# Kernel optimization log

Hardware: AMD Instinct MI355X
Metric: run time of the kernel (lower is better)

Reference implementation:

```python
import jax, jax.numpy as jnp
import numpy as np

G = 10            # int(2 / 0.2) BEV grid side
NUM_PILLARS = G * G
INTERVAL = 0.2
BN_EPS = 1e-5


def setup_inputs() -> dict:
    key = jax.random.key(0)
    ks = jax.random.split(key, 8)
    B, N = 8, 20000
    x = jax.random.normal(ks[0], (B, N, 3), dtype=jnp.float32)
    # Linear weights stored as [in, out] (torch Linear applies x @ W.T); no biases.
    W1 = jax.random.normal(ks[1], (6, 32), dtype=jnp.float32) * 0.1
    W2 = jax.random.normal(ks[2], (32, 64), dtype=jnp.float32) * 0.1
    W3 = jax.random.normal(ks[3], (64, 128), dtype=jnp.float32) * 0.1
    W4 = jax.random.normal(ks[4], (256, 768), dtype=jnp.float32) * 0.05
    bn_gamma = jnp.ones((NUM_PILLARS,), dtype=jnp.float32)
    bn_beta = jnp.zeros((NUM_PILLARS,), dtype=jnp.float32)
    return {"x": x, "W1": W1, "W2": W2, "W3": W3, "W4": W4,
            "bn_gamma": bn_gamma, "bn_beta": bn_beta}


def _encode_sample(p, seg, W1, W2, W3, W4):
    # p: [N,3] swapped coords (Z,Y,X); seg: [N] pillar id in [0,100)
    N = p.shape[0]
    counts = jax.ops.segment_sum(jnp.ones((N,), p.dtype), seg, num_segments=NUM_PILLARS)  # [100]
    cent = jax.ops.segment_sum(p, seg, num_segments=NUM_PILLARS) / jnp.maximum(counts, 1.0)[:, None]
    aug = jnp.concatenate([p, p - cent[seg]], axis=-1)          # [N,6]
    h = jax.nn.relu(aug @ W1)
    h = jax.nn.relu(h @ W2)
    h = jax.nn.relu(h @ W3)                                      # [N,128]
    pil = jax.ops.segment_max(h, seg, num_segments=NUM_PILLARS)  # [100,128] (-inf on empty, never gathered)
    h2 = jnp.concatenate([h, pil[seg]], axis=-1)                 # [N,256]
    h2 = jax.nn.relu(h2 @ W4)                                    # [N,768]
    enc = jax.ops.segment_max(h2, seg, num_segments=NUM_PILLARS) # [100,768]
    return jnp.where(counts[:, None] > 0, enc, 0.0)             # empty pillars stay zero


def reference(x, W1, W2, W3, W4, bn_gamma, bn_beta):
    # column swap [Y,Z,X] -> [Z,Y,X]
    pts = jnp.stack([x[..., 1], x[..., 0], x[..., 2]], axis=-1)  # [B,N,3]
    # pillar indices from (Y, X) = swapped cols 1:3
    yx = jnp.clip(pts[..., 1:] + 1.0, 0.0, 1.99)
    idx = jnp.floor(yx / INTERVAL).astype(jnp.int32)             # trunc == floor (non-negative)
    seg = idx[..., 0] * G + idx[..., 1]                          # [B,N], matches flatten(2) order y*10+x
    feat = jax.vmap(lambda p, s: _encode_sample(p, s, W1, W2, W3, W4))(pts, seg)  # [B,100,768]
    # BatchNorm1d(100) in training mode over [B, 100, 768]: stats over dims (0,2)
    mean = feat.mean(axis=(0, 2))
    var = feat.var(axis=(0, 2))  # biased variance, as torch uses for normalization
    out = (feat - mean[None, :, None]) * jax.lax.rsqrt(var + BN_EPS)[None, :, None]
    return out * bn_gamma[None, :, None] + bn_beta[None, :, None]
```

## Files before the change

### kernel.cpp

```cpp
#include <hip/hip_runtime.h>
#include <stdint.h>

#define B_    8
#define N_    20000
#define NPTS  (B_*N_)
#define G_    10
#define NPIL  100
#define NSB   (B_*NPIL)
#define BN_EPS 1e-5f

#define OFF_COUNTS   0
#define OFF_SUMS     3200
#define OFF_STARTS   12800
#define OFF_ZPAD     16064
#define ZERO_BYTES   16320
#define OFF_CENT     19264
#define OFF_SEG      28864
#define OFF_W3BF     668864
#define OFF_W4T      709824
#define OFF_PILBF    1103040
#define OFF_PILW4B   1307840
#define OFF_H3P      3765440
#define WS_NEED      44725440

typedef __attribute__((ext_vector_type(8))) short bf16x8;
typedef __attribute__((ext_vector_type(4))) float f32x4;

typedef const __attribute__((address_space(1))) void gas_void;
typedef __attribute__((address_space(3))) void las_void;

__device__ __forceinline__ void gload_lds16(const void* g, void* l){
    __builtin_amdgcn_global_load_lds((gas_void*)g, (las_void*)l, 16, 0, 0);
}

__device__ __forceinline__ int binidx(float v){
    float t = v + 1.0f;
    t = fminf(fmaxf(t, 0.0f), 1.99f);
    return (int)(t / 0.2f);
}
__device__ __forceinline__ unsigned short f2bf(float f){
    unsigned u = __float_as_uint(f);
    u += 0x7fffu + ((u >> 16) & 1u);
    return (unsigned short)(u >> 16);
}
__device__ __forceinline__ unsigned u16max2(unsigned a, unsigned b){
    unsigned ah=a>>16, bh=b>>16, al=a&0xffffu, bl=b&0xffffu;
    return ((ah>bh?ah:bh)<<16) | (al>bl?al:bl);
}
__device__ __forceinline__ uint4 max16(uint4 a, uint4 b){
    uint4 r; r.x=u16max2(a.x,b.x); r.y=u16max2(a.y,b.y);
    r.z=u16max2(a.z,b.z); r.w=u16max2(a.w,b.w); return r;
}

__global__ __launch_bounds__(256) void kA(const float* __restrict__ x,
                                          int* __restrict__ segrank,
                                          int* __restrict__ counts,
                                          float* __restrict__ sums){
    __shared__ int   lc[NSB];
    __shared__ float lsum[NSB*3];
    __shared__ int   lbase[NSB];
    int tid = threadIdx.x;
    for (int j = tid; j < NSB; j += 256){
        lc[j] = 0;
        lsum[3*j] = 0.f; lsum[3*j+1] = 0.f; lsum[3*j+2] = 0.f;
    }
    __syncthreads();
    int i0 = blockIdx.x * 625;
    int sbv[3], lrv[3];
    #pragma unroll
    for (int t = 0; t < 3; t++){
        int i = i0 + tid + t*256;
        sbv[t] = -1;
        if (tid + t*256 < 625 && i < NPTS){
            float x0 = x[3*i], x1 = x[3*i+1], x2 = x[3*i+2];
            int b  = i / N_;
            int sb = b*NPIL + binidx(x0)*G_ + binidx(x2);
            sbv[t] = sb;
            lrv[t] = atomicAdd(&lc[sb], 1);
            atomicAdd(&lsum[sb*3+0], x1);
            atomicAdd(&lsum[sb*3+1], x0);
            atomicAdd(&lsum[sb*3+2], x2);
        }
    }
    __syncthreads();
    for (int j = tid; j < NSB; j += 256){
        int c = lc[j];
        if (c > 0){
            lbase[j] = atomicAdd(&counts[j], c);
            atomicAdd(&sums[3*j+0], lsum[3*j+0]);
            atomicAdd(&sums[3*j+1], lsum[3*j+1]);
            atomicAdd(&sums[3*j+2], lsum[3*j+2]);
        }
    }
    __syncthreads();
    #pragma unroll
    for (int t = 0; t < 3; t++){
        if (sbv[t] >= 0){
            int i = i0 + tid + t*256;
            int rank = lbase[sbv[t]] + lrv[t];
            segrank[i] = sbv[t] | (rank << 10);
        }
    }
}

__global__ __launch_bounds__(1024) void kScan(const int* __restrict__ counts,
                                              int* __restrict__ starts){
    __shared__ int s[1024];
    int t = threadIdx.x;
    int c = (t < NSB) ? counts[t] : 0;
    s[t] = c;
    __syncthreads();
    for (int off=1; off<1024; off<<=1){
        int v = (t >= off) ? s[t-off] : 0;
        __syncthreads();
        s[t] += v;
        __syncthreads();
    }
    if (t < NSB) starts[t] = s[t]-c;
    if (t == NSB) starts[NSB] = s[NSB-1];
}

__global__ __launch_bounds__(256) void kB(const int* __restrict__ counts,
                                          const float* __restrict__ sums,
                                          float* __restrict__ cent,
                                          const float* __restrict__ W3,
                                          unsigned short* __restrict__ W3bf,
                                          const float* __restrict__ W4,
                                          unsigned short* __restrict__ W4T){
    int idx = blockIdx.x*256 + threadIdx.x;
    if (idx < 2400){
        cent[idx] = sums[idx] / fmaxf((float)counts[idx/3], 1.0f);
    } else if (idx < 2400 + 8192){
        int t = idx - 2400;
        int col = t >> 6, k = t & 63;
        W3bf[t] = f2bf(W3[k*128 + col]);
    } else if (idx < 2400 + 8192 + 196608){
        int t = idx - 2400 - 8192;
        int k = t / 768, j = t - k*768;
        W4T[j*256 + k] = f2bf(W4[t]);
    }
}

__global__ __launch_bounds__(256) void kC12(const float* __restrict__ x,
                                            const int* __restrict__ segrank,
                                            const int* __restrict__ starts,
                                            const float* __restrict__ cent,
                                            const float* __restrict__ W1,
                                            const float* __restrict__ W2,
                                            unsigned short* __restrict__ h3p){
    int i = blockIdx.x*256 + threadIdx.x;
    if (i >= NPTS) return;
    int pk = segrank[i];
    int sb = pk & 1023;
    int pos = starts[sb] + (pk >> 10);
    float p0 = x[3*i+1], p1 = x[3*i], p2 = x[3*i+2];
    float aug[6];
    aug[0]=p0; aug[1]=p1; aug[2]=p2;
    aug[3]=p0-cent[sb*3+0]; aug[4]=p1-cent[sb*3+1]; aug[5]=p2-cent[sb*3+2];

    float h1[32];
    #pragma unroll
    for (int j=0;j<32;j++){
        float a = 0.f;
        #pragma unroll
        for (int k=0;k<6;k++) a += aug[k]*W1[k*32+j];
        h1[j] = fmaxf(a, 0.f);
    }
    unsigned buf[32];
    #pragma unroll 8
    for (int jp=0;jp<32;jp++){
        float a0 = 0.f, a1 = 0.f;
        #pragma unroll
        for (int k=0;k<32;k++){
            a0 += h1[k]*W2[k*64 + jp*2];
            a1 += h1[k]*W2[k*64 + jp*2 + 1];
        }
        buf[jp] = (unsigned)f2bf(fmaxf(a0,0.f)) | ((unsigned)f2bf(fmaxf(a1,0.f)) << 16);
    }
    uint4* d4 = (uint4*)(h3p + (size_t)pos*128 + 64);
    #pragma unroll
    for (int q=0;q<8;q++) d4[q] = ((const uint4*)buf)[q];
}

__global__ __launch_bounds__(512) void kC3(const unsigned short* __restrict__ W3bf,
                                           unsigned short* __restrict__ h3p){
    __shared__ unsigned short Al[256*64];
    __shared__ unsigned short Bl[128*64];
    int tid = threadIdx.x;
    int m0  = blockIdx.x * 256;
    #pragma unroll
    for (int it=0; it<4; it++){
        int cc = tid + it*512;
        int row = cc >> 3, ch = cc & 7;
        int chs = ch ^ (row & 7);
        gload_lds16(h3p + (size_t)(m0+row)*128 + 64 + chs*8, (char*)Al + cc*16);
    }
    #pragma unroll
    for (int it=0; it<2; it++){
        int cc = tid + it*512;
        int row = cc >> 3, ch = cc & 7;
        int chs = ch ^ (row & 7);
        gload_lds16(W3bf + (size_t)row*64 + chs*8, (char*)Bl + cc*16);
    }
    __syncthreads();

    int lane = tid & 63, wid = tid >> 6;
    int wm = wid >> 1, wn = wid & 1;
    int l15 = lane & 15, lhi = lane >> 4;

    f32x4 acc[4][4];
    #pragma unroll
    for (int m=0;m<4;m++)
        #pragma unroll
        for (int n=0;n<4;n++) acc[m][n] = (f32x4){0.f,0.f,0.f,0.f};

    #pragma unroll
    for (int kk=0; kk<2; kk++){
        bf16x8 af[4], bfr[4];
        #pragma unroll
        for (int f=0; f<4; f++){
            int ra = wm*64 + f*16 + l15;
            af[f]  = *(const bf16x8*)((char*)Al + ra*128 + (((kk*4+lhi) ^ (ra&7))*16));
            int rb = wn*64 + f*16 + l15;
            bfr[f] = *(const bf16x8*)((char*)Bl + rb*128 + (((kk*4+lhi) ^ (rb&7))*16));
        }
        #pragma unroll
        for (int m=0;m<4;m++)
            #pragma unroll
            for (int n=0;n<4;n++)
                acc[m][n] = __builtin_amdgcn_mfma_f32_16x16x32_bf16(af[m], bfr[n], acc[m][n], 0,0,0);
    }

    #pragma unroll
    for (int m=0;m<4;m++)
        #pragma unroll
        for (int r=0;r<4;r++){
            int row = m0 + wm*64 + m*16 + lhi*4 + r;
            #pragma unroll
            for (int n=0;n<4;n++){
                int col = wn*64 + n*16 + l15;
                h3p[(size_t)row*128 + col] = f2bf(fmaxf(acc[m][n][r], 0.f));
            }
        }
}

__global__ __launch_bounds__(256) void kM(const unsigned short* __restrict__ h3p,
                                          const int* __restrict__ starts,
                                          unsigned short* __restrict__ pilbf){
    __shared__ uint4 sd[16][16];
    int sb = blockIdx.x;
    int tx = threadIdx.x & 15, ty = threadIdx.x >> 4;
    int s = starts[sb], npts = starts[sb+1] - s;
    uint4 acc = {0u,0u,0u,0u};
    for (int p = ty; p < npts; p += 16){
        uint4 v = *(const uint4*)(h3p + (size_t)(s+p)*128 + tx*8);
        acc = max16(acc, v);
    }
    sd[ty][tx] = acc;
    __syncthreads();
    #pragma unroll
    for (int off=8; off; off>>=1){
        if (ty < off) sd[ty][tx] = max16(sd[ty][tx], sd[ty+off][tx]);
        __syncthreads();
    }
    if (ty == 0) *(uint4*)(pilbf + sb*128 + tx*8) = sd[0][tx];
}

__global__ __launch_bounds__(256) void kPB(const unsigned short* __restrict__ pilbf,
                                           const unsigned short* __restrict__ W4T,
                                           float* __restrict__ pilW4b){
    __shared__ unsigned short Al[128*128];
    __shared__ unsigned short Bl[128*128];
    int m0 = blockIdx.x * 128;
    int n0 = blockIdx.y * 128;
    int tid = threadIdx.x;
    #pragma unroll
    for (int it=0; it<8; it++){
        int cc = tid + it*256;
        int row = cc >> 4, ch = cc & 15;
        int chs = ch ^ (row & 7);
        uint4 v = {0u,0u,0u,0u};
        if (m0 + row < NSB) v = *(const uint4*)(pilbf + (size_t)(m0+row)*128 + chs*8);
        *(uint4*)((char*)Al + cc*16) = v;
        uint4 vb = *(const uint4*)(W4T + (size_t)(n0+row)*256 + 128 + chs*8);
        *(uint4*)((char*)Bl + cc*16) = vb;
    }
    __syncthreads();
    int lane = tid & 63, wid = tid >> 6;
    int wm = wid >> 1, wn = wid & 1;
    int l15 = lane & 15, lhi = lane >> 4;
    f32x4 acc[4][4];
    #pragma unroll
    for (int m=0;m<4;m++)
        #pragma unroll
        for (int n=0;n<4;n++) acc[m][n] = (f32x4){0.f,0.f,0.f,0.f};
    #pragma unroll
    for (int kk=0; kk<4; kk++){
        bf16x8 af[4], bfr[4];
        #pragma unroll
        for (int f=0; f<4; f++){
            int ra = wm*64 + f*16 + l15;
            af[f]  = *(const bf16x8*)((char*)Al + ra*256 + (((kk*4+lhi) ^ (ra&7))*16));
            int rb = wn*64 + f*16 + l15;
            bfr[f] = *(const bf16x8*)((char*)Bl + rb*256 + (((kk*4+lhi) ^ (rb&7))*16));
        }
        #pragma unroll
        for (int m=0;m<4;m++)
            #pragma unroll
            for (int n=0;n<4;n++)
                acc[m][n] = __builtin_amdgcn_mfma_f32_16x16x32_bf16(af[m], bfr[n], acc[m][n], 0,0,0);
    }
    #pragma unroll
    for (int m=0;m<4;m++)
        #pragma unroll
        for (int r=0;r<4;r++){
            int p = wm*64 + m*16 + lhi*4 + r;
            int sbp = m0 + p;
            if (sbp < NSB){
                #pragma unroll
                for (int n=0;n<4;n++)
                    pilW4b[(size_t)sbp*768 + n0 + wn*64 + n*16 + l15] = acc[m][n][r];
            }
        }
}

__global__ __launch_bounds__(256) void kD(const unsigned short* __restrict__ h3p,
                                          const unsigned short* __restrict__ zpad,
                                          const int* __restrict__ starts,
                                          const float* __restrict__ pilW4b,
                                          const unsigned short* __restrict__ W4T,
                                          float* __restrict__ out){
    __shared__ unsigned short Al[128*128];
    __shared__ unsigned short Bl[128*128];
    __shared__ float red[2][2][64];
    int b  = blockIdx.x;
    int x_ = b & 7, t_ = b >> 3;
    int k_ = t_ / 6, nt = t_ - k_*6;
    int sb = x_ + 8*k_;
    int n0 = nt * 128;
    int tid = threadIdx.x;
    int start = starts[sb];
    int npts  = starts[sb+1] - start;
    if (npts == 0){
        if (tid < 128) out[(size_t)sb*768 + n0 + tid] = 0.f;
        return;
    }
    #pragma unroll
    for (int it=0; it<8; it++){
        int cc = tid + it*256;
        int row = cc >> 4, ch = cc & 15;
        int chs = ch ^ (row & 7);
        gload_lds16(W4T + (size_t)(n0+row)*256 + chs*8, (char*)Bl + cc*16);
    }
    int lane = tid & 63, wid = tid >> 6;
    int wm = wid >> 1, wn = wid & 1;
    int l15 = lane & 15, lhi = lane >> 4;

    float bias[4];
    #pragma unroll
    for (int n=0;n<4;n++) bias[n] = pilW4b[(size_t)sb*768 + n0 + wn*64 + n*16 + l15];

    float mx[4][4][4];
    #pragma unroll
    for (int m=0;m<4;m++)
        #pragma unroll
        for (int n=0;n<4;n++)
            #pragma unroll
            for (int r=0;r<4;r++) mx[m][n][r] = 0.f;

    int nch = (npts + 127) >> 7;
    for (int c=0; c<nch; c++){
        int base = c*128;
        __syncthreads();
        #pragma unroll
        for (int it=0; it<8; it++){
            int cc = tid + it*256;
            int row = cc >> 4, ch = cc & 15;
            int chs = ch ^ (row & 7);
            const unsigned short* src = (base + row < npts)
                ? h3p + (size_t)(start+base+row)*128 + chs*8
                : zpad + chs*8;
            gload_lds16(src, (char*)Al + cc*16);
        }
        __syncthreads();

        f32x4 acc[4][4];
        #pragma unroll
        for (int m=0;m<4;m++)
            #pragma unroll
            for (int n=0;n<4;n++) acc[m][n] = (f32x4){0.f,0.f,0.f,0.f};

        #pragma unroll
        for (int kk=0; kk<4; kk++){
            bf16x8 af[4], bfr[4];
            #pragma unroll
            for (int f=0; f<4; f++){
                int ra = wm*64 + f*16 + l15;
                af[f]  = *(const bf16x8*)((char*)Al + ra*256 + (((kk*4+lhi) ^ (ra&7))*16));
                int rb = wn*64 + f*16 + l15;
                bfr[f] = *(const bf16x8*)((char*)Bl + rb*256 + (((kk*4+lhi) ^ (rb&7))*16));
            }
            #pragma unroll
            for (int m=0;m<4;m++)
                #pragma unroll
                for (int n=0;n<4;n++)
                    acc[m][n] = __builtin_amdgcn_mfma_f32_16x16x32_bf16(af[m], bfr[n], acc[m][n], 0,0,0);
        }

        int nrem = npts - base;
        #pragma unroll
        for (int m=0;m<4;m++)
            #pragma unroll
            for (int r=0;r<4;r++){
                int p = wm*64 + m*16 + lhi*4 + r;
                if (p < nrem){
                    #pragma unroll
                    for (int n=0;n<4;n++)
                        mx[m][n][r] = fmaxf(mx[m][n][r], fmaxf(acc[m][n][r] + bias[n], 0.f));
                }
            }
    }

    float red4[4];
    #pragma unroll
    for (int n=0;n<4;n++){
        float v = 0.f;
        #pragma unroll
        for (int m=0;m<4;m++)
            #pragma unroll
            for (int r=0;r<4;r++) v = fmaxf(v, mx[m][n][r]);
        v = fmaxf(v, __shfl_xor(v, 16));
        v = fmaxf(v, __shfl_xor(v, 32));
        red4[n] = v;
    }
    if (lhi == 0){
        #pragma unroll
        for (int n=0;n<4;n++) red[wm][wn][n*16 + l15] = red4[n];
    }
    __syncthreads();
    if (wm == 0){
        float v = fmaxf(red[0][wn][lane], red[1][wn][lane]);
        out[(size_t)sb*768 + n0 + wn*64 + lane] = v;
    }
}

__global__ __launch_bounds__(256) void kE(float* __restrict__ out,
                                          const float* __restrict__ gamma,
                                          const float* __restrict__ beta){
    int p = blockIdx.x;
    int tid = threadIdx.x;
    float v[B_*3];
    float sum = 0.f, ssq = 0.f;
    #pragma unroll
    for (int b=0;b<B_;b++)
        #pragma unroll
        for (int r=0;r<3;r++){
            float t = out[(b*NPIL + p)*768 + tid + r*256];
            v[b*3+r] = t;
            sum += t; ssq += t*t;
        }
    #pragma unroll
    for (int off=32; off; off>>=1){
        sum += __shfl_xor(sum, off);
        ssq += __shfl_xor(ssq, off);
    }
    __shared__ float ls[8];
    __shared__ float sc[2];
    int lane = tid & 63, w = tid >> 6;
    if (lane == 0){ ls[w] = sum; ls[4+w] = ssq; }
    __syncthreads();
    if (tid == 0){
        float S = ls[0]+ls[1]+ls[2]+ls[3];
        float Q = ls[4]+ls[5]+ls[6]+ls[7];
        float mean = S * (1.0f/6144.0f);
        float var  = Q * (1.0f/6144.0f) - mean*mean;
        float scale = rsqrtf(var + BN_EPS) * gamma[p];
        sc[0] = scale;
        sc[1] = beta[p] - mean*scale;
    }
    __syncthreads();
    float scale = sc[0], shift = sc[1];
    #pragma unroll
    for (int b=0;b<B_;b++)
        #pragma unroll
        for (int r=0;r<3;r++)
            out[(b*NPIL + p)*768 + tid + r*256] = v[b*3+r]*scale + shift;
}

extern "C" void kernel_launch(void* const* d_in, const int* in_sizes, int n_in,
                              void* d_out, int out_size, void* d_ws, size_t ws_size,
                              hipStream_t stream){
    if (ws_size < (size_t)WS_NEED) return;
    const float* x     = (const float*)d_in[0];
    const float* W1    = (const float*)d_in[1];
    const float* W2    = (const float*)d_in[2];
    const float* W3    = (const float*)d_in[3];
    const float* W4    = (const float*)d_in[4];
    const float* gamma = (const float*)d_in[5];
    const float* beta  = (const float*)d_in[6];
    float* out = (float*)d_out;
    char*  ws  = (char*)d_ws;

    int*            counts = (int*)           (ws + OFF_COUNTS);
    float*          sums   = (float*)         (ws + OFF_SUMS);
    int*            starts = (int*)           (ws + OFF_STARTS);
    unsigned short* zpad   = (unsigned short*)(ws + OFF_ZPAD);
    float*          cent   = (float*)         (ws + OFF_CENT);
    int*            segrank= (int*)           (ws + OFF_SEG);
    unsigned short* W3bf   = (unsigned short*)(ws + OFF_W3BF);
    unsigned short* W4T    = (unsigned short*)(ws + OFF_W4T);
    unsigned short* pilbf  = (unsigned short*)(ws + OFF_PILBF);
    float*          pilW4b = (float*)         (ws + OFF_PILW4B);
    unsigned short* h3p    = (unsigned short*)(ws + OFF_H3P);

    hipMemsetAsync(d_ws, 0, ZERO_BYTES, stream);

    kA<<<256, 256, 0, stream>>>(x, segrank, counts, sums);
    kScan<<<1, 1024, 0, stream>>>(counts, starts);
    kB<<<(2400+8192+196608+255)/256, 256, 0, stream>>>(counts, sums, cent, W3, W3bf, W4, W4T);
    kC12<<<(NPTS+255)/256, 256, 0, stream>>>(x, segrank, starts, cent, W1, W2, h3p);
    kC3<<<NPTS/256, 512, 0, stream>>>(W3bf, h3p);
    kM<<<NSB, 256, 0, stream>>>(h3p, starts, pilbf);
    dim3 gPB((NSB+127)/128, 6);
    kPB<<<gPB, 256, 0, stream>>>(pilbf, W4T, pilW4b);
    kD<<<4800, 256, 0, stream>>>(h3p, zpad, starts, pilW4b, W4T, out);
    kE<<<NPIL, 256, 0, stream>>>(out, gamma, beta);
}
```

Before: 175.7 us.

## Fuse layer-3 MFMA into per-point MLP kernel and pillar max/bias into kD

Merges the per-point layer 1-2 kernel with the layer-3 MFMA GEMM, so the 64-wide intermediate goes through LDS and no longer round-trips through h3p in global memory. It also drops the separate pillar segment-max and pillar-bias GEMM kernels. Each kD block now recomputes the pillar max over its points and a 128-column slice of the pillar·W4 bias in scalar code. This removes three launches and global round trips, but the 6 column-tile blocks per pillar repeat the max reduction and bias dot products, and the fused kernel raises register and LDS use.

```diff
diff --git a/kernel.cpp b/kernel.cpp
--- a/kernel.cpp
+++ b/kernel.cpp
@@ -18,8 +18,6 @@
 #define OFF_SEG      28864
 #define OFF_W3BF     668864
 #define OFF_W4T      709824
-#define OFF_PILBF    1103040
-#define OFF_PILW4B   1307840
 #define OFF_H3P      3765440
 #define WS_NEED      44725440
 
@@ -141,18 +139,33 @@
     }
 }
 
-__global__ __launch_bounds__(256) void kC12(const float* __restrict__ x,
-                                            const int* __restrict__ segrank,
-                                            const int* __restrict__ starts,
-                                            const float* __restrict__ cent,
-                                            const float* __restrict__ W1,
-                                            const float* __restrict__ W2,
-                                            unsigned short* __restrict__ h3p){
-    int i = blockIdx.x*256 + threadIdx.x;
-    if (i >= NPTS) return;
+__global__ __launch_bounds__(256) void kCF(const float* __restrict__ x,
+                                           const int* __restrict__ segrank,
+                                           const int* __restrict__ starts,
+                                           const float* __restrict__ cent,
+                                           const float* __restrict__ W1,
+                                           const float* __restrict__ W2,
+                                           const unsigned short* __restrict__ W3bf,
+                                           unsigned short* __restrict__ h3p){
+    __shared__ uint4 Hl4[256*8];
+    __shared__ uint4 Bw4[128*8];
+    __shared__ int posl[256];
+    unsigned short* Hl = (unsigned short*)Hl4;
+    unsigned short* Bw = (unsigned short*)Bw4;
+    int tid = threadIdx.x;
+    int i = blockIdx.x*256 + tid;
     int pk = segrank[i];
     int sb = pk & 1023;
-    int pos = starts[sb] + (pk >> 10);
+    posl[tid] = starts[sb] + (pk >> 10);
+
+    #pragma unroll
+    for (int it=0; it<4; it++){
+        int cc = tid + it*256;
+        int row = cc >> 3, ch = cc & 7;
+        int chs = ch ^ (row & 7);
+        gload_lds16(W3bf + (size_t)row*64 + chs*8, (char*)Bw + cc*16);
+    }
+
     float p0 = x[3*i+1], p1 = x[3*i], p2 = x[3*i+2];
     float aug[6];
     aug[0]=p0; aug[1]=p1; aug[2]=p2;
@@ -166,7 +179,7 @@
         for (int k=0;k<6;k++) a += aug[k]*W1[k*32+j];
         h1[j] = fmaxf(a, 0.f);
     }
-    unsigned buf[32];
+    unsigned buf[32] __attribute__((aligned(16)));
     #pragma unroll 8
     for (int jp=0;jp<32;jp++){
         float a0 = 0.f, a1 = 0.f;
@@ -177,30 +190,10 @@
         }
         buf[jp] = (unsigned)f2bf(fmaxf(a0,0.f)) | ((unsigned)f2bf(fmaxf(a1,0.f)) << 16);
     }
-    uint4* d4 = (uint4*)(h3p + (size_t)pos*128 + 64);
-    #pragma unroll
-    for (int q=0;q<8;q++) d4[q] = ((const uint4*)buf)[q];
-}
-
-__global__ __launch_bounds__(512) void kC3(const unsigned short* __restrict__ W3bf,
-                                           unsigned short* __restrict__ h3p){
-    __shared__ unsigned short Al[256*64];
-    __shared__ unsigned short Bl[128*64];
-    int tid = threadIdx.x;
-    int m0  = blockIdx.x * 256;
-    #pragma unroll
-    for (int it=0; it<4; it++){
-        int cc = tid + it*512;
-        int row = cc >> 3, ch = cc & 7;
-        int chs = ch ^ (row & 7);
-        gload_lds16(h3p + (size_t)(m0+row)*128 + 64 + chs*8, (char*)Al + cc*16);
-    }
-    #pragma unroll
-    for (int it=0; it<2; it++){
-        int cc = tid + it*512;
-        int row = cc >> 3, ch = cc & 7;
-        int chs = ch ^ (row & 7);
-        gload_lds16(W3bf + (size_t)row*64 + chs*8, (char*)Bl + cc*16);
+    #pragma unroll
+    for (int ch=0; ch<8; ch++){
+        int chs = ch ^ (tid & 7);
+        *(uint4*)((char*)Hl + tid*128 + chs*16) = ((const uint4*)buf)[ch];
     }
     __syncthreads();
 
@@ -208,131 +201,56 @@
     int wm = wid >> 1, wn = wid & 1;
     int l15 = lane & 15, lhi = lane >> 4;
 
-    f32x4 acc[4][4];
-    #pragma unroll
-    for (int m=0;m<4;m++)
-        #pragma unroll
-        for (int n=0;n<4;n++) acc[m][n] = (f32x4){0.f,0.f,0.f,0.f};
+    f32x4 acc[8][4];
+    #pragma unroll
+    for (int f=0;f<8;f++)
+        #pragma unroll
+        for (int n=0;n<4;n++) acc[f][n] = (f32x4){0.f,0.f,0.f,0.f};
 
     #pragma unroll
     for (int kk=0; kk<2; kk++){
-        bf16x8 af[4], bfr[4];
-        #pragma unroll
-        for (int f=0; f<4; f++){
-            int ra = wm*64 + f*16 + l15;
-            af[f]  = *(const bf16x8*)((char*)Al + ra*128 + (((kk*4+lhi) ^ (ra&7))*16));
-            int rb = wn*64 + f*16 + l15;
-            bfr[f] = *(const bf16x8*)((char*)Bl + rb*128 + (((kk*4+lhi) ^ (rb&7))*16));
-        }
-        #pragma unroll
-        for (int m=0;m<4;m++)
+        bf16x8 af[8], bfr[4];
+        #pragma unroll
+        for (int f=0; f<8; f++){
+            int ra = wm*128 + f*16 + l15;
+            af[f] = *(const bf16x8*)((char*)Hl + ra*128 + (((kk*4+lhi) ^ (ra&7))*16));
+        }
+        #pragma unroll
+        for (int n=0; n<4; n++){
+            int rb = wn*64 + n*16 + l15;
+            bfr[n] = *(const bf16x8*)((char*)Bw + rb*128 + (((kk*4+lhi) ^ (rb&7))*16));
+        }
+        #pragma unroll
+        for (int f=0;f<8;f++)
             #pragma unroll
             for (int n=0;n<4;n++)
-                acc[m][n] = __builtin_amdgcn_mfma_f32_16x16x32_bf16(af[m], bfr[n], acc[m][n], 0,0,0);
-    }
-
-    #pragma unroll
-    for (int m=0;m<4;m++)
+                acc[f][n] = __builtin_amdgcn_mfma_f32_16x16x32_bf16(af[f], bfr[n], acc[f][n], 0,0,0);
+    }
+
+    #pragma unroll
+    for (int f=0;f<8;f++)
         #pragma unroll
         for (int r=0;r<4;r++){
-            int row = m0 + wm*64 + m*16 + lhi*4 + r;
-            #pragma unroll
-            for (int n=0;n<4;n++){
-                int col = wn*64 + n*16 + l15;
-                h3p[(size_t)row*128 + col] = f2bf(fmaxf(acc[m][n][r], 0.f));
-            }
-        }
-}
-
-__global__ __launch_bounds__(256) void kM(const unsigned short* __restrict__ h3p,
-                                          const int* __restrict__ starts,
-                                          unsigned short* __restrict__ pilbf){
-    __shared__ uint4 sd[16][16];
-    int sb = blockIdx.x;
-    int tx = threadIdx.x & 15, ty = threadIdx.x >> 4;
-    int s = starts[sb], npts = starts[sb+1] - s;
-    uint4 acc = {0u,0u,0u,0u};
-    for (int p = ty; p < npts; p += 16){
-        uint4 v = *(const uint4*)(h3p + (size_t)(s+p)*128 + tx*8);
-        acc = max16(acc, v);
-    }
-    sd[ty][tx] = acc;
-    __syncthreads();
-    #pragma unroll
-    for (int off=8; off; off>>=1){
-        if (ty < off) sd[ty][tx] = max16(sd[ty][tx], sd[ty+off][tx]);
-        __syncthreads();
-    }
-    if (ty == 0) *(uint4*)(pilbf + sb*128 + tx*8) = sd[0][tx];
-}
-
-__global__ __launch_bounds__(256) void kPB(const unsigned short* __restrict__ pilbf,
-                                           const unsigned short* __restrict__ W4T,
-                                           float* __restrict__ pilW4b){
-    __shared__ unsigned short Al[128*128];
-    __shared__ unsigned short Bl[128*128];
-    int m0 = blockIdx.x * 128;
-    int n0 = blockIdx.y * 128;
-    int tid = threadIdx.x;
-    #pragma unroll
-    for (int it=0; it<8; it++){
-        int cc = tid + it*256;
-        int row = cc >> 4, ch = cc & 15;
-        int chs = ch ^ (row & 7);
-        uint4 v = {0u,0u,0u,0u};
-        if (m0 + row < NSB) v = *(const uint4*)(pilbf + (size_t)(m0+row)*128 + chs*8);
-        *(uint4*)((char*)Al + cc*16) = v;
-        uint4 vb = *(const uint4*)(W4T + (size_t)(n0+row)*256 + 128 + chs*8);
-        *(uint4*)((char*)Bl + cc*16) = vb;
-    }
-    __syncthreads();
-    int lane = tid & 63, wid = tid >> 6;
-    int wm = wid >> 1, wn = wid & 1;
-    int l15 = lane & 15, lhi = lane >> 4;
-    f32x4 acc[4][4];
-    #pragma unroll
-    for (int m=0;m<4;m++)
-        #pragma unroll
-        for (int n=0;n<4;n++) acc[m][n] = (f32x4){0.f,0.f,0.f,0.f};
-    #pragma unroll
-    for (int kk=0; kk<4; kk++){
-        bf16x8 af[4], bfr[4];
-        #pragma unroll
-        for (int f=0; f<4; f++){
-            int ra = wm*64 + f*16 + l15;
-            af[f]  = *(const bf16x8*)((char*)Al + ra*256 + (((kk*4+lhi) ^ (ra&7))*16));
-            int rb = wn*64 + f*16 + l15;
-            bfr[f] = *(const bf16x8*)((char*)Bl + rb*256 + (((kk*4+lhi) ^ (rb&7))*16));
-        }
-        #pragma unroll
-        for (int m=0;m<4;m++)
+            int row = wm*128 + f*16 + lhi*4 + r;
+            int pos = posl[row];
+            unsigned short* orow = h3p + (size_t)pos*128 + wn*64 + l15;
             #pragma unroll
             for (int n=0;n<4;n++)
-                acc[m][n] = __builtin_amdgcn_mfma_f32_16x16x32_bf16(af[m], bfr[n], acc[m][n], 0,0,0);
-    }
-    #pragma unroll
-    for (int m=0;m<4;m++)
-        #pragma unroll
-        for (int r=0;r<4;r++){
-            int p = wm*64 + m*16 + lhi*4 + r;
-            int sbp = m0 + p;
-            if (sbp < NSB){
-                #pragma unroll
-                for (int n=0;n<4;n++)
-                    pilW4b[(size_t)sbp*768 + n0 + wn*64 + n*16 + l15] = acc[m][n][r];
-            }
+                orow[n*16] = f2bf(fmaxf(acc[f][n][r], 0.f));
         }
 }
 
 __global__ __launch_bounds__(256) void kD(const unsigned short* __restrict__ h3p,
                                           const unsigned short* __restrict__ zpad,
                                           const int* __restrict__ starts,
-                                          const float* __restrict__ pilW4b,
                                           const unsigned short* __restrict__ W4T,
                                           float* __restrict__ out){
     __shared__ unsigned short Al[128*128];
     __shared__ unsigned short Bl[128*128];
     __shared__ float red[2][2][64];
+    __shared__ uint4 pill4[16];
+    __shared__ float biasl[128];
+    unsigned short* pill = (unsigned short*)pill4;
     int b  = blockIdx.x;
     int x_ = b & 7, t_ = b >> 3;
     int k_ = t_ / 6, nt = t_ - k_*6;
@@ -352,13 +270,52 @@
         int chs = ch ^ (row & 7);
         gload_lds16(W4T + (size_t)(n0+row)*256 + chs*8, (char*)Bl + cc*16);
     }
+    int tx = tid & 15, ty = tid >> 4;
+    uint4 mx4 = {0u,0u,0u,0u};
+    for (int p = ty; p < npts; p += 16)
+        mx4 = max16(mx4, *(const uint4*)(h3p + (size_t)(start+p)*128 + tx*8));
+    uint4* sc = (uint4*)Al;
+    sc[ty*16+tx] = mx4;
+    __syncthreads();
+    #pragma unroll
+    for (int off=8; off; off>>=1){
+        if (ty < off) sc[ty*16+tx] = max16(sc[ty*16+tx], sc[(ty+off)*16+tx]);
+        __syncthreads();
+    }
+    if (tid < 16) pill4[tid] = sc[tid];
+    __syncthreads();
+    if (tid < 128){
+        const unsigned short* wrow = W4T + (size_t)(n0+tid)*256 + 128;
+        float s = 0.f;
+        #pragma unroll
+        for (int q=0;q<16;q++){
+            uint4 wv = *(const uint4*)(wrow + q*8);
+            uint4 pv = pill4[q >> 1];
+            const unsigned* w2 = (const unsigned*)&wv;
+            const unsigned* p2a = (const unsigned*)&pv;
+            const unsigned* p2 = p2a + (q & 1)*2;
+            #pragma unroll
+            for (int e=0;e<4;e++){
+                unsigned pw = ((const unsigned*)&pill4[q>>1])[ (q&1)*2 + (e>>1) ];
+                (void)p2; (void)pw;
+            }
+            const unsigned short* pl = pill + q*8;
+            const unsigned short* wl = (const unsigned short*)&wv;
+            #pragma unroll
+            for (int e=0;e<8;e++)
+                s += __uint_as_float(((unsigned)wl[e])<<16) * __uint_as_float(((unsigned)pl[e])<<16);
+        }
+        biasl[tid] = s;
+    }
+    __syncthreads();
+
     int lane = tid & 63, wid = tid >> 6;
     int wm = wid >> 1, wn = wid & 1;
     int l15 = lane & 15, lhi = lane >> 4;
 
     float bias[4];
     #pragma unroll
-    for (int n=0;n<4;n++) bias[n] = pilW4b[(size_t)sb*768 + n0 + wn*64 + n*16 + l15];
+    for (int n=0;n<4;n++) bias[n] = biasl[wn*64 + n*16 + l15];
 
     float mx[4][4][4];
     #pragma unroll
@@ -509,8 +466,6 @@
     int*            segrank= (int*)           (ws + OFF_SEG);
     unsigned short* W3bf   = (unsigned short*)(ws + OFF_W3BF);
     unsigned short* W4T    = (unsigned short*)(ws + OFF_W4T);
-    unsigned short* pilbf  = (unsigned short*)(ws + OFF_PILBF);
-    float*          pilW4b = (float*)         (ws + OFF_PILW4B);
     unsigned short* h3p    = (unsigned short*)(ws + OFF_H3P);
 
     hipMemsetAsync(d_ws, 0, ZERO_BYTES, stream);
@@ -518,11 +473,7 @@
     kA<<<256, 256, 0, stream>>>(x, segrank, counts, sums);
     kScan<<<1, 1024, 0, stream>>>(counts, starts);
     kB<<<(2400+8192+196608+255)/256, 256, 0, stream>>>(counts, sums, cent, W3, W3bf, W4, W4T);
-    kC12<<<(NPTS+255)/256, 256, 0, stream>>>(x, segrank, starts, cent, W1, W2, h3p);
-    kC3<<<NPTS/256, 512, 0, stream>>>(W3bf, h3p);
-    kM<<<NSB, 256, 0, stream>>>(h3p, starts, pilbf);
-    dim3 gPB((NSB+127)/128, 6);
-    kPB<<<gPB, 256, 0, stream>>>(pilbf, W4T, pilW4b);
-    kD<<<4800, 256, 0, stream>>>(h3p, zpad, starts, pilW4b, W4T, out);
+    kCF<<<NPTS/256, 256, 0, stream>>>(x, segrank, starts, cent, W1, W2, W3bf, h3p);
+    kD<<<4800, 256, 0, stream>>>(h3p, zpad, starts, W4T, out);
     kE<<<NPIL, 256, 0, stream>>>(out, gamma, beta);
 }
```

Measured after the change: 228.6 us. 30.1% more time.
